# Kernel optimization log

Measured on AMD Instinct MI355X. Metric: run time of the kernel, lower is better.

The kernel has to match this reference:

```python
import jax, jax.numpy as jnp
import numpy as np


def setup_inputs() -> dict:
    key = jax.random.key(0)
    k1, k2 = jax.random.split(key)
    B, N, C, P = 256, 196, 3, 16
    x = jax.random.normal(k1, (B, N, C, P, P), dtype=jnp.float32)
    # Conv2d(C, 1, kernel=P, stride=P) weight, squeezed to [C, P, P]
    W = jax.random.normal(k2, (C, P, P), dtype=jnp.float32) * (1.0 / np.sqrt(C * P * P))
    b = jnp.zeros((1,), dtype=jnp.float32)
    return {"x": x, "W": W, "b": b}


def reference(x, W, b):
    # kernel_size == stride == patch size and each patch is exactly P x P,
    # so the per-patch conv is a single dot product over (C, P, P) plus bias.
    # output: [B, N]
    return jnp.einsum("bnchw,chw->bn", x, W) + b[0]
```

## Files before the change

kernel.cpp:

```cpp
#include <hip/hip_runtime.h>

__global__ __launch_bounds__(256) void patchconv_kernel(
    const float* __restrict__ x,
    const float* __restrict__ W,
    const float* __restrict__ b,
    float* __restrict__ out,
    int nrows) {
  const int gtid = blockIdx.x * blockDim.x + threadIdx.x;
  const int wave = gtid >> 6;
  const int lane = threadIdx.x & 63;
  if (wave >= nrows) return;

  const float4* __restrict__ xr =
      reinterpret_cast<const float4*>(x + (size_t)wave * 768);
  const float4* __restrict__ wr = reinterpret_cast<const float4*>(W);

  float sum = 0.f;
#pragma unroll
  for (int k = 0; k < 3; ++k) {
    const float4 xv = xr[lane + k * 64];
    const float4 wv = wr[lane + k * 64];
    sum += xv.x * wv.x + xv.y * wv.y + xv.z * wv.z + xv.w * wv.w;
  }

#pragma unroll
  for (int off = 32; off > 0; off >>= 1)
    sum += __shfl_down(sum, off, 64);

  if (lane == 0) out[wave] = sum + b[0];
}

extern "C" void kernel_launch(void* const* d_in, const int* in_sizes, int n_in,
                              void* d_out, int out_size, void* d_ws, size_t ws_size,
                              hipStream_t stream) {
  const float* x = (const float*)d_in[0];
  const float* W = (const float*)d_in[1];
  const float* b = (const float*)d_in[2];
  float* out = (float*)d_out;

  const int nrows = out_size;
  const int wavesPerBlock = 4;
  const int blocks = (nrows + wavesPerBlock - 1) / wavesPerBlock;
  patchconv_kernel<<<blocks, 256, 0, stream>>>(x, W, b, out, nrows);
}
```

Baseline: 26.90 us.

## Process eight rows per wave with butterfly transpose-reduce

Each wave now computes eight output rows instead of one. It loads W once into registers and issues eight row loads per chunk to raise memory-level parallelism. The eight partial sums are combined with a select-and-xor-shuffle butterfly, so one set of shuffles reduces all rows. The cost is higher register use and fewer waves in flight for a kernel that is already bandwidth-bound.

```diff
diff --git a/kernel.cpp b/kernel.cpp
--- a/kernel.cpp
+++ b/kernel.cpp
@@ -1,6 +1,8 @@
 #include <hip/hip_runtime.h>
 
-__global__ __launch_bounds__(256) void patchconv_kernel(
+constexpr int ROWS = 8;
+
+__global__ __launch_bounds__(256, 6) void patchconv_kernel(
     const float* __restrict__ x,
     const float* __restrict__ W,
     const float* __restrict__ b,
@@ -9,25 +11,56 @@
   const int gtid = blockIdx.x * blockDim.x + threadIdx.x;
   const int wave = gtid >> 6;
   const int lane = threadIdx.x & 63;
-  if (wave >= nrows) return;
+  const int base = wave * ROWS;
+  if (base >= nrows) return;
+
+  const float4* __restrict__ wr = reinterpret_cast<const float4*>(W);
+  float4 wv[3];
+#pragma unroll
+  for (int k = 0; k < 3; ++k) wv[k] = wr[lane + k * 64];
+
+  float sums[ROWS];
+#pragma unroll
+  for (int r = 0; r < ROWS; ++r) sums[r] = 0.f;
 
   const float4* __restrict__ xr =
-      reinterpret_cast<const float4*>(x + (size_t)wave * 768);
-  const float4* __restrict__ wr = reinterpret_cast<const float4*>(W);
+      reinterpret_cast<const float4*>(x + (size_t)base * 768);
 
-  float sum = 0.f;
 #pragma unroll
   for (int k = 0; k < 3; ++k) {
-    const float4 xv = xr[lane + k * 64];
-    const float4 wv = wr[lane + k * 64];
-    sum += xv.x * wv.x + xv.y * wv.y + xv.z * wv.z + xv.w * wv.w;
+    float4 xv[ROWS];
+#pragma unroll
+    for (int r = 0; r < ROWS; ++r) xv[r] = xr[r * 192 + k * 64 + lane];
+#pragma unroll
+    for (int r = 0; r < ROWS; ++r) {
+      sums[r] += xv[r].x * wv[k].x + xv[r].y * wv[k].y +
+                 xv[r].z * wv[k].z + xv[r].w * wv[k].w;
+    }
   }
 
-#pragma unroll
-  for (int off = 32; off > 0; off >>= 1)
-    sum += __shfl_down(sum, off, 64);
+  auto merge = [&](float a, float bb, int mask) -> float {
+    const bool up = (lane & mask) != 0;
+    const float sel = up ? a : bb;
+    const float got = __shfl_xor(sel, mask, 64);
+    const float mine = up ? bb : a;
+    return mine + got;
+  };
 
-  if (lane == 0) out[wave] = sum + b[0];
+  float m0 = merge(sums[0], sums[4], 32);
+  float m1 = merge(sums[1], sums[5], 32);
+  float m2 = merge(sums[2], sums[6], 32);
+  float m3 = merge(sums[3], sums[7], 32);
+  float n0 = merge(m0, m1, 16);
+  float n1 = merge(m2, m3, 16);
+  float p  = merge(n0, n1, 8);
+  p += __shfl_xor(p, 4, 64);
+  p += __shfl_xor(p, 2, 64);
+  p += __shfl_xor(p, 1, 64);
+
+  if ((lane & 7) == 0) {
+    const int idx = 4 * ((lane >> 5) & 1) + ((lane >> 4) & 1) + 2 * ((lane >> 3) & 1);
+    if (base + idx < nrows) out[base + idx] = p + b[0];
+  }
 }
 
 extern "C" void kernel_launch(void* const* d_in, const int* in_sizes, int n_in,
@@ -39,7 +72,7 @@
   float* out = (float*)d_out;
 
   const int nrows = out_size;
-  const int wavesPerBlock = 4;
-  const int blocks = (nrows + wavesPerBlock - 1) / wavesPerBlock;
+  const int wavesNeeded = (nrows + ROWS - 1) / ROWS;
+  const int blocks = (wavesNeeded + 3) / 4;
   patchconv_kernel<<<blocks, 256, 0, stream>>>(x, W, b, out, nrows);
 }
```

New measurement: 27.39 us. Within noise of the previous version (+1.8%).
